# Kernel tuning notes

Measured on AMD Instinct MI355X. Metric: run time of the kernel, lower is better.

## Reference

```python
import jax, jax.numpy as jnp
from jax import lax
import numpy as np

EPS = 1e-3  # Keras BatchNormalization default epsilon
G, B, H, W, CIN, BF, COUT = 32, 16, 56, 56, 128, 4, 256


def _bn_relu(x, g, b, m, v):
    return jax.nn.relu((x - m) * lax.rsqrt(v + EPS) * g + b)


def _conv(x, w, stride):
    # x: NHWC, w: HWIO
    return lax.conv_general_dilated(x, w, (stride, stride), 'VALID',
                                    dimension_numbers=('NHWC', 'HWIO', 'NHWC'))


def _forward(x, params):
    # params: 18-tuple of per-branch stacked tensors, leading dim G=32
    cout = params[-1].shape[-1]
    b, h, w, _ = x.shape
    out_shape = (b, h // 2, w // 2, cout)

    def step(acc, p):
        g1, be1, m1, v1, w1, bb1, g2, be2, m2, v2, w3, bb3, g3, be3, m3, v3, w2, bb2 = p
        t = _bn_relu(x, g1, be1, m1, v1)
        t = _conv(t, w1, 1) + bb1                      # [B,H,W,4]
        t = _bn_relu(t, g2, be2, m2, v2)
        t = jnp.pad(t, ((0, 0), (1, 1), (1, 1), (0, 0)))
        t = _conv(t, w3, 2) + bb3                      # [B,H/2,W/2,4]
        t = _bn_relu(t, g3, be3, m3, v3)
        t = _conv(t, w2, 1) + bb2                      # [B,H/2,W/2,Cout]
        return acc + t, None

    y, _ = lax.scan(step, jnp.zeros(out_shape, x.dtype), params)
    # frozen 1x1 stride-2 downsample conv with ones kernel, zero bias:
    # each output channel equals the channel-sum of the strided input.
    res = jnp.sum(x[:, ::2, ::2, :], axis=-1, keepdims=True)  # [B,H/2,W/2,1]
    return y + res


def setup_inputs() -> dict:
    key = jax.random.key(0)
    ks = jax.random.split(key, 19)
    sc = 0.05  # he-normal-ish small init for conv kernels
    return {
        'x': jax.random.normal(ks[0], (B, H, W, CIN), jnp.float32),
        'bn1_gamma': jax.random.uniform(ks[1], (G, CIN), jnp.float32, 0.5, 1.5),
        'bn1_beta': jax.random.normal(ks[2], (G, CIN), jnp.float32) * 0.1,
        'bn1_mean': jax.random.normal(ks[3], (G, CIN), jnp.float32) * 0.1,
        'bn1_var': jax.random.uniform(ks[4], (G, CIN), jnp.float32, 0.5, 1.5),
        'W1': jax.random.normal(ks[5], (G, 1, 1, CIN, BF), jnp.float32) * sc,
        'b1': jax.random.normal(ks[6], (G, BF), jnp.float32) * sc,
        'bn2_gamma': jax.random.uniform(ks[7], (G, BF), jnp.float32, 0.5, 1.5),
        'bn2_beta': jax.random.normal(ks[8], (G, BF), jnp.float32) * 0.1,
        'bn2_mean': jax.random.normal(ks[9], (G, BF), jnp.float32) * 0.1,
        'bn2_var': jax.random.uniform(ks[10], (G, BF), jnp.float32, 0.5, 1.5),
        'W3': jax.random.normal(ks[11], (G, 3, 3, BF, BF), jnp.float32) * sc,
        'b3': jax.random.normal(ks[12], (G, BF), jnp.float32) * sc,
        'bn3_gamma': jax.random.uniform(ks[13], (G, BF), jnp.float32, 0.5, 1.5),
        'bn3_beta': jax.random.normal(ks[14], (G, BF), jnp.float32) * 0.1,
        'bn3_mean': jax.random.normal(ks[15], (G, BF), jnp.float32) * 0.1,
        'bn3_var': jax.random.uniform(ks[16], (G, BF), jnp.float32, 0.5, 1.5),
        'W2': jax.random.normal(ks[17], (G, 1, 1, BF, COUT), jnp.float32) * sc,
        'b2': jax.random.normal(ks[18], (G, COUT), jnp.float32) * sc,
    }


def reference(x, bn1_gamma, bn1_beta, bn1_mean, bn1_var, W1, b1,
              bn2_gamma, bn2_beta, bn2_mean, bn2_var, W3, b3,
              bn3_gamma, bn3_beta, bn3_mean, bn3_var, W2, b2):
    params = (bn1_gamma, bn1_beta, bn1_mean, bn1_var, W1, b1,
              bn2_gamma, bn2_beta, bn2_mean, bn2_var, W3, b3,
              bn3_gamma, bn3_beta, bn3_mean, bn3_var, W2, b2)
    return _forward(x, params)
```

## Files before the change

kernel.cpp:

```cpp
#include <hip/hip_runtime.h>
#include <hip/hip_bf16.h>

#define EPS 1e-3f
#define NPIX  50176
#define NOPIX 12544

#define OFF_S2   0
#define OFF_T2   128
#define OFF_T3   256
#define OFF_BSUM 384
#define OFF_W3S  640
#define OFF_TPH  5248
#define OFF_WAF  7296
#define OFF_U    40064
#define OFF_V    3251328

typedef __attribute__((ext_vector_type(4))) float f32x4;
typedef __attribute__((ext_vector_type(8))) _Float16 f16x8;
typedef __attribute__((ext_vector_type(4))) _Float16 f16x4;

__device__ __forceinline__ unsigned short f2bf(float f) {
    unsigned u = __float_as_uint(f);
    return (unsigned short)((u + 0x7fffu + ((u >> 16) & 1u)) >> 16);
}
__device__ __forceinline__ float bf2f(unsigned short s) {
    return __uint_as_float(((unsigned)s) << 16);
}
__device__ __forceinline__ unsigned pk2bf(float lo, float hi) {
    __hip_bfloat162 p = __float22bfloat162_rn(make_float2(lo, hi));
    union { __hip_bfloat162 h; unsigned u; } c; c.h = p;
    return c.u;
}
__device__ __forceinline__ unsigned short f2h(float f) {
    union { _Float16 h; unsigned short u; } c;
    c.h = (_Float16)f;
    return c.u;
}

__global__ __launch_bounds__(256)
void prep_kernel(const float* __restrict__ g1, const float* __restrict__ be1,
                 const float* __restrict__ m1, const float* __restrict__ v1,
                 const float* __restrict__ W1, const float* __restrict__ b1,
                 const float* __restrict__ g2, const float* __restrict__ be2,
                 const float* __restrict__ m2, const float* __restrict__ v2,
                 const float* __restrict__ W3, const float* __restrict__ b3,
                 const float* __restrict__ g3, const float* __restrict__ be3,
                 const float* __restrict__ m3, const float* __restrict__ v3,
                 const float* __restrict__ b2, float* __restrict__ ws) {
    int gid = blockIdx.x * 256 + threadIdx.x;
    int stride = gridDim.x * 256;
    {
        unsigned short* tph = (unsigned short*)(ws + OFF_TPH);
        for (int i = gid; i < 4096; i += stride) {
            int j  = i & 7, lq = (i >> 3) & 3, kk = (i >> 5) & 3, g = i >> 7;
            int c = kk*32 + lq*8 + j;
            float s = g1[g*128 + c] * rsqrtf(v1[g*128 + c] + EPS);
            tph[i] = f2h(be1[g*128 + c] / s - m1[g*128 + c]);
        }
    }
    {
        unsigned short* wsu = (unsigned short*)(ws + OFF_WAF);
        for (int i = gid; i < 65536; i += stride) {
            int j    = i & 7;
            int lane = (i >> 3) & 63;
            int kk   = (i >> 9) & 3;
            int g    = i >> 11;
            int f    = lane & 15;
            int c    = kk*32 + (lane >> 4)*8 + j;
            unsigned short v = 0;
            if (f < 4) {
                float s = g1[g*128 + c] * rsqrtf(v1[g*128 + c] + EPS);
                v = f2h(s * W1[g*512 + c*4 + f]);
            }
            wsu[i] = v;
        }
    }
    for (int i = gid; i < 4608; i += stride) {
        int k = i / 36, j = i - k*36;
        int kk = j >> 2, ci = j & 3;
        int g = k >> 2, f = k & 3;
        float s3 = g3[k] * rsqrtf(v3[k] + EPS);
        ws[OFF_W3S + i] = W3[g*144 + kk*16 + ci*4 + f] * s3;
    }
    if (gid < 128) {
        float s2 = g2[gid] * rsqrtf(v2[gid] + EPS);
        ws[OFF_S2 + gid] = s2;
        ws[OFF_T2 + gid] = be2[gid] + (b1[gid] - m2[gid]) * s2;
        float s3 = g3[gid] * rsqrtf(v3[gid] + EPS);
        ws[OFF_T3 + gid] = be3[gid] + (b3[gid] - m3[gid]) * s3;
    } else if (gid >= 256 && gid < 512) {
        int co = gid - 256;
        float acc = 0.f;
        for (int g = 0; g < 32; ++g) acc += b2[g*256 + co];
        ws[OFF_BSUM + co] = acc;
    }
}

__global__ __launch_bounds__(512, 4)
void stage1_kernel(const float* __restrict__ x,
                   const float* __restrict__ tabs,
                   float* __restrict__ uout) {
    __shared__ uint4 xs[1024];
    int tid = threadIdx.x;
    int tile  = blockIdx.x >> 1;
    int ghalf = blockIdx.x & 1;

    {
        const float4* xg = (const float4*)x + (size_t)tile * 2048;
        #pragma unroll
        for (int r = 0; r < 4; ++r) {
            int i = tid + 512*r;
            int px = i >> 5, c4 = i & 31;
            float4 v = xg[i];
            union { f16x4 h; uint2 u; } hv;
            hv.h = (f16x4){(_Float16)v.x, (_Float16)v.y, (_Float16)v.z, (_Float16)v.w};
            int cc = c4 >> 1, hf = c4 & 1;
            ((uint2*)xs)[(px*16 + (cc ^ (px & 15)))*2 + hf] = hv.u;
        }
    }

    int lane = tid & 63;
    int wid  = tid >> 6;
    int g0   = __builtin_amdgcn_readfirstlane(ghalf*16 + wid*2);
    int l15  = lane & 15;
    int lq   = lane >> 4;

    union U4H { uint4 u; f16x8 h; };
    U4H af[2][4];
    {
        const uint4* wafp = (const uint4*)(tabs + OFF_WAF);
        #pragma unroll
        for (int gi = 0; gi < 2; ++gi)
            #pragma unroll
            for (int kk = 0; kk < 4; ++kk)
                af[gi][kk].u = wafp[((g0 + gi)*4 + kk)*64 + lane];
    }
    U4H tph[2][4];
    {
        const uint4* tphp = (const uint4*)(tabs + OFF_TPH);
        #pragma unroll
        for (int gi = 0; gi < 2; ++gi)
            #pragma unroll
            for (int kk = 0; kk < 4; ++kk)
                tph[gi][kk].u = tphp[((g0 + gi)*4 + kk)*4 + lq];
    }
    __syncthreads();

    uint2* Uo = (uint2*)uout;
    const f32x4 zro = {0.f, 0.f, 0.f, 0.f};
    const f16x8 zh = {0, 0, 0, 0, 0, 0, 0, 0};

    #pragma unroll 1
    for (int t = 0; t < 4; ++t) {
        int pxl = t*16 + l15;
        U4H xf[4];
        #pragma unroll
        for (int kk = 0; kk < 4; ++kk)
            xf[kk].u = xs[pxl*16 + ((kk*4 + lq) ^ (pxl & 15))];
        #pragma unroll
        for (int gi = 0; gi < 2; ++gi) {
            int g = g0 + gi;
            f32x4 acc = zro;
            #pragma unroll
            for (int kk = 0; kk < 4; ++kk) {
                f16x8 z = __builtin_elementwise_max(xf[kk].h + tph[gi][kk].h, zh);
                acc = __builtin_amdgcn_mfma_f32_16x16x32_f16(af[gi][kk].h, z, acc, 0, 0, 0);
            }
            const float4 s2v = ((const float4*)(tabs + OFF_S2))[g];
            const float4 t2v = ((const float4*)(tabs + OFF_T2))[g];
            float o0 = fmaxf(fmaf(acc[0], s2v.x, t2v.x), 0.f);
            float o1 = fmaxf(fmaf(acc[1], s2v.y, t2v.y), 0.f);
            float o2 = fmaxf(fmaf(acc[2], s2v.z, t2v.z), 0.f);
            float o3 = fmaxf(fmaf(acc[3], s2v.w, t2v.w), 0.f);
            uint2 val;
            val.x = pk2bf(o0, o1);
            val.y = pk2bf(o2, o3);
            if (lane < 16)
                Uo[(size_t)g * NPIX + tile*64 + t*16 + lane] = val;
        }
    }
}

__global__ __launch_bounds__(256)
void stage2a_kernel(const float* __restrict__ tabs,
                    const float* __restrict__ U,
                    float* __restrict__ V) {
    __shared__ ushort4 patch[3*16*32];

    int tid = threadIdx.x;
    int row = blockIdx.x >> 2;
    int q   = blockIdx.x & 3;
    int b = row / 28, oh = row - b*28;

    {
        const ushort4* Uu = (const ushort4*)U;
        #pragma unroll 1
        for (int i = tid; i < 1440; i += 256) {
            int g = i / 45;
            int rem = i - g*45;
            int r = rem / 15;
            int c = rem - r*15;
            int ih = 2*oh - 1 + r;
            int ic = 14*q - 1 + c;
            ushort4 v = make_ushort4(0, 0, 0, 0);
            if (ih >= 0 && ic >= 0)
                v = Uu[(size_t)g * NPIX + (b*56 + ih)*56 + ic];
            patch[(r*16 + c)*32 + (g ^ c)] = v;
        }
    }

    int k = tid & 127, s = tid >> 7;
    int g = k >> 2;
    float4 w[9];
    {
        const float4* wk = (const float4*)(tabs + OFF_W3S + k*36);
        #pragma unroll
        for (int kk = 0; kk < 9; ++kk) w[kk] = wk[kk];
    }
    float t3 = tabs[OFF_T3 + k];
    __syncthreads();

    #pragma unroll
    for (int j = 0; j < 4; ++j) {
        int opx_l = s + 2*j;
        if (opx_l > 6) break;
        float acc = 0.f;
        #pragma unroll
        for (int kh = 0; kh < 3; ++kh) {
            #pragma unroll
            for (int kw = 0; kw < 3; ++kw) {
                int cc = 2*opx_l + kw;
                ushort4 u = patch[(kh*16 + cc)*32 + (g ^ cc)];
                float4 wv = w[kh*3 + kw];
                acc = fmaf(bf2f(u.x), wv.x, acc);
                acc = fmaf(bf2f(u.y), wv.y, acc);
                acc = fmaf(bf2f(u.z), wv.z, acc);
                acc = fmaf(bf2f(u.w), wv.w, acc);
            }
        }
        int opx = row*28 + q*7 + opx_l;
        V[(size_t)opx*128 + k] = fmaxf(acc + t3, 0.f);
    }
}

__global__ __launch_bounds__(256)
void stage2b_kernel(const float* __restrict__ x,
                    const float* __restrict__ W2,
                    const float* __restrict__ tabs,
                    const float* __restrict__ V,
                    float* __restrict__ out) {
    __shared__ float vs[8*128];
    __shared__ float res_s[8];
    int tid = threadIdx.x;
    int opxBase = blockIdx.x * 8;

    {
        const float* Vb = V + (size_t)opxBase * 128;
        #pragma unroll
        for (int jj = 0; jj < 4; ++jj) vs[tid + 256*jj] = Vb[tid + 256*jj];
    }
    {
        int p = tid >> 5, l = tid & 31;
        int opx = opxBase + p;
        int b = opx / 784, r = opx - b*784;
        int oh = r / 28, ow = r - oh*28;
        const float* xp = x + (size_t)((b*56 + 2*oh)*56 + 2*ow) * 128;
        float rv = xp[l] + xp[l+32] + xp[l+64] + xp[l+96];
        #pragma unroll
        for (int off = 16; off; off >>= 1) rv += __shfl_down(rv, off, 32);
        if (l == 0) res_s[p] = rv;
    }
    __syncthreads();

    int co = tid;
    float acc[8];
    {
        float bs = tabs[OFF_BSUM + co];
        #pragma unroll
        for (int p = 0; p < 8; ++p) acc[p] = bs;
    }
    const float* W2c = W2 + co;
    #pragma unroll 4
    for (int k4 = 0; k4 < 32; ++k4) {
        float w0 = W2c[(4*k4+0)*256];
        float w1 = W2c[(4*k4+1)*256];
        float w2 = W2c[(4*k4+2)*256];
        float w3 = W2c[(4*k4+3)*256];
        #pragma unroll
        for (int p = 0; p < 8; ++p) {
            float4 v = *(const float4*)&vs[p*128 + k4*4];
            acc[p] = fmaf(v.x, w0, acc[p]);
            acc[p] = fmaf(v.y, w1, acc[p]);
            acc[p] = fmaf(v.z, w2, acc[p]);
            acc[p] = fmaf(v.w, w3, acc[p]);
        }
    }
    #pragma unroll
    for (int p = 0; p < 8; ++p)
        out[(size_t)(opxBase + p)*256 + co] = acc[p] + res_s[p];
}

extern "C" void kernel_launch(void* const* d_in, const int* in_sizes, int n_in,
                              void* d_out, int out_size, void* d_ws, size_t ws_size,
                              hipStream_t stream) {
    const float* x   = (const float*)d_in[0];
    const float* g1  = (const float*)d_in[1];
    const float* be1 = (const float*)d_in[2];
    const float* m1  = (const float*)d_in[3];
    const float* v1  = (const float*)d_in[4];
    const float* W1  = (const float*)d_in[5];
    const float* b1  = (const float*)d_in[6];
    const float* g2  = (const float*)d_in[7];
    const float* be2 = (const float*)d_in[8];
    const float* m2  = (const float*)d_in[9];
    const float* v2  = (const float*)d_in[10];
    const float* W3  = (const float*)d_in[11];
    const float* b3  = (const float*)d_in[12];
    const float* g3  = (const float*)d_in[13];
    const float* be3 = (const float*)d_in[14];
    const float* m3  = (const float*)d_in[15];
    const float* v3  = (const float*)d_in[16];
    const float* W2  = (const float*)d_in[17];
    const float* b2  = (const float*)d_in[18];
    float* out = (float*)d_out;
    float* ws  = (float*)d_ws;

    prep_kernel<<<64, 256, 0, stream>>>(g1, be1, m1, v1, W1, b1, g2, be2, m2,
                                        v2, W3, b3, g3, be3, m3, v3, b2, ws);
    stage1_kernel<<<(NPIX / 64) * 2, 512, 0, stream>>>(x, ws, ws + OFF_U);
    stage2a_kernel<<<448 * 4, 256, 0, stream>>>(ws, ws + OFF_U, ws + OFF_V);
    stage2b_kernel<<<NOPIX / 8, 256, 0, stream>>>(x, W2, ws, ws + OFF_V, out);
}
```

Baseline: 156.0 us.

## Fuse grouped 3x3 conv and 1x1 expansion conv into one stage2 kernel

```diff
diff --git a/kernel.cpp b/kernel.cpp
--- a/kernel.cpp
+++ b/kernel.cpp
@@ -13,7 +13,6 @@
 #define OFF_TPH  5248
 #define OFF_WAF  7296
 #define OFF_U    40064
-#define OFF_V    3251328
 
 typedef __attribute__((ext_vector_type(4))) float f32x4;
 typedef __attribute__((ext_vector_type(8))) _Float16 f16x8;
@@ -182,30 +181,48 @@
 }
 
 __global__ __launch_bounds__(256)
-void stage2a_kernel(const float* __restrict__ tabs,
-                    const float* __restrict__ U,
-                    float* __restrict__ V) {
-    __shared__ ushort4 patch[3*16*32];
+void stage2_kernel(const float* __restrict__ x,
+                   const float* __restrict__ W2,
+                   const float* __restrict__ tabs,
+                   const float* __restrict__ U,
+                   float* __restrict__ out) {
+    __shared__ ushort4 patch[3*30*32];
+    __shared__ float vs[14*128];
+    __shared__ float res_s[14];
 
     int tid = threadIdx.x;
-    int row = blockIdx.x >> 2;
-    int q   = blockIdx.x & 3;
+    int row = blockIdx.x >> 1;
+    int qh  = blockIdx.x & 1;
     int b = row / 28, oh = row - b*28;
 
     {
         const ushort4* Uu = (const ushort4*)U;
         #pragma unroll 1
-        for (int i = tid; i < 1440; i += 256) {
-            int g = i / 45;
-            int rem = i - g*45;
-            int r = rem / 15;
-            int c = rem - r*15;
+        for (int i = tid; i < 2880; i += 256) {
+            int g = i / 90;
+            int rem = i - g*90;
+            int r = rem / 30;
+            int c = rem - r*30;
             int ih = 2*oh - 1 + r;
-            int ic = 14*q - 1 + c;
+            int ic = 28*qh - 1 + c;
             ushort4 v = make_ushort4(0, 0, 0, 0);
-            if (ih >= 0 && ic >= 0)
+            if (ih >= 0 && ic >= 0 && ic < 56)
                 v = Uu[(size_t)g * NPIX + (b*56 + ih)*56 + ic];
-            patch[(r*16 + c)*32 + (g ^ c)] = v;
+            patch[(r*30 + c)*32 + (g ^ c)] = v;
+        }
+    }
+
+    {
+        int p = tid >> 4, l = tid & 15;
+        if (p < 14) {
+            int ow = qh*14 + p;
+            const float* xp = x + (size_t)((b*56 + 2*oh)*56 + 2*ow) * 128 + l;
+            float rv = 0.f;
+            #pragma unroll
+            for (int c = 0; c < 8; ++c) rv += xp[c*16];
+            #pragma unroll
+            for (int off = 8; off; off >>= 1) rv += __shfl_down(rv, off, 16);
+            if (l == 0) res_s[p] = rv;
         }
     }
 
@@ -220,17 +237,16 @@
     float t3 = tabs[OFF_T3 + k];
     __syncthreads();
 
-    #pragma unroll
-    for (int j = 0; j < 4; ++j) {
+    #pragma unroll 1
+    for (int j = 0; j < 7; ++j) {
         int opx_l = s + 2*j;
-        if (opx_l > 6) break;
         float acc = 0.f;
         #pragma unroll
         for (int kh = 0; kh < 3; ++kh) {
             #pragma unroll
             for (int kw = 0; kw < 3; ++kw) {
                 int cc = 2*opx_l + kw;
-                ushort4 u = patch[(kh*16 + cc)*32 + (g ^ cc)];
+                ushort4 u = patch[(kh*30 + cc)*32 + (g ^ cc)];
                 float4 wv = w[kh*3 + kw];
                 acc = fmaf(bf2f(u.x), wv.x, acc);
                 acc = fmaf(bf2f(u.y), wv.y, acc);
@@ -238,46 +254,16 @@
                 acc = fmaf(bf2f(u.w), wv.w, acc);
             }
         }
-        int opx = row*28 + q*7 + opx_l;
-        V[(size_t)opx*128 + k] = fmaxf(acc + t3, 0.f);
-    }
-}
-
-__global__ __launch_bounds__(256)
-void stage2b_kernel(const float* __restrict__ x,
-                    const float* __restrict__ W2,
-                    const float* __restrict__ tabs,
-                    const float* __restrict__ V,
-                    float* __restrict__ out) {
-    __shared__ float vs[8*128];
-    __shared__ float res_s[8];
-    int tid = threadIdx.x;
-    int opxBase = blockIdx.x * 8;
-
-    {
-        const float* Vb = V + (size_t)opxBase * 128;
-        #pragma unroll
-        for (int jj = 0; jj < 4; ++jj) vs[tid + 256*jj] = Vb[tid + 256*jj];
-    }
-    {
-        int p = tid >> 5, l = tid & 31;
-        int opx = opxBase + p;
-        int b = opx / 784, r = opx - b*784;
-        int oh = r / 28, ow = r - oh*28;
-        const float* xp = x + (size_t)((b*56 + 2*oh)*56 + 2*ow) * 128;
-        float rv = xp[l] + xp[l+32] + xp[l+64] + xp[l+96];
-        #pragma unroll
-        for (int off = 16; off; off >>= 1) rv += __shfl_down(rv, off, 32);
-        if (l == 0) res_s[p] = rv;
+        vs[opx_l*128 + k] = fmaxf(acc + t3, 0.f);
     }
     __syncthreads();
 
     int co = tid;
-    float acc[8];
+    float acc[14];
     {
         float bs = tabs[OFF_BSUM + co];
         #pragma unroll
-        for (int p = 0; p < 8; ++p) acc[p] = bs;
+        for (int p = 0; p < 14; ++p) acc[p] = bs;
     }
     const float* W2c = W2 + co;
     #pragma unroll 4
@@ -287,7 +273,7 @@
         float w2 = W2c[(4*k4+2)*256];
         float w3 = W2c[(4*k4+3)*256];
         #pragma unroll
-        for (int p = 0; p < 8; ++p) {
+        for (int p = 0; p < 14; ++p) {
             float4 v = *(const float4*)&vs[p*128 + k4*4];
             acc[p] = fmaf(v.x, w0, acc[p]);
             acc[p] = fmaf(v.y, w1, acc[p]);
@@ -295,9 +281,10 @@
             acc[p] = fmaf(v.w, w3, acc[p]);
         }
     }
+    size_t obase = ((size_t)row * 28 + qh*14) * 256;
     #pragma unroll
-    for (int p = 0; p < 8; ++p)
-        out[(size_t)(opxBase + p)*256 + co] = acc[p] + res_s[p];
+    for (int p = 0; p < 14; ++p)
+        out[obase + (size_t)p*256 + co] = acc[p] + res_s[p];
 }
 
 extern "C" void kernel_launch(void* const* d_in, const int* in_sizes, int n_in,
@@ -328,6 +315,5 @@
     prep_kernel<<<64, 256, 0, stream>>>(g1, be1, m1, v1, W1, b1, g2, be2, m2,
                                         v2, W3, b3, g3, be3, m3, v3, b2, ws);
     stage1_kernel<<<(NPIX / 64) * 2, 512, 0, stream>>>(x, ws, ws + OFF_U);
-    stage2a_kernel<<<448 * 4, 256, 0, stream>>>(ws, ws + OFF_U, ws + OFF_V);
-    stage2b_kernel<<<NOPIX / 8, 256, 0, stream>>>(x, W2, ws, ws + OFF_V, out);
-}
+    stage2_kernel<<<448 * 2, 256, 0, stream>>>(x, W2, ws, ws + OFF_U, out);
+}
```

New measurement: 155.3 us. No clear change (-0.5%).
